# Kernel optimization log

Measured on AMD Instinct MI355X. Metric: run time of the kernel, lower is better.

The kernel has to match this reference:

```python
import jax, jax.numpy as jnp
import numpy as np

D_MODEL = 256
N_HEADS = 8
HEAD_DIM = D_MODEL // N_HEADS


def setup_inputs() -> dict:
    key = jax.random.key(0)
    k1, k2, k3, k4, k5, k6, k7 = jax.random.split(key, 7)
    B, T, N, D = 4, 32, 32, D_MODEL
    x = jax.random.normal(k1, (B, T, N, D), dtype=jnp.float32)
    bias_features = jax.random.normal(k2, (B, T, N, N, D), dtype=jnp.float32)
    # alive mask, mostly True so rows are rarely fully masked
    mask = jax.random.uniform(k3, (B, T, N)) < 0.9
    s = 1.0 / np.sqrt(D)
    w_qkv = jax.random.normal(k4, (D, 3 * D), dtype=jnp.float32) * s
    b_qkv = jnp.zeros((3 * D,), dtype=jnp.float32)
    w_proj = jax.random.normal(k5, (D, D), dtype=jnp.float32) * s
    b_proj = jnp.zeros((D,), dtype=jnp.float32)
    return {"x": x, "bias_features": bias_features, "mask": mask,
            "w_qkv": w_qkv, "b_qkv": b_qkv, "w_proj": w_proj, "b_proj": b_proj}


def reference(x, bias_features, mask, w_qkv, b_qkv, w_proj, b_proj):
    B, T, N, D = x.shape
    H, Dh = N_HEADS, D // N_HEADS
    Bt = B * T
    xf = x.reshape(Bt, N, D)
    qkv = xf @ w_qkv + b_qkv                       # (Bt, N, 3D)
    q, k, v = jnp.split(qkv, 3, axis=-1)
    q = q.reshape(Bt, N, H, Dh)
    k = k.reshape(Bt, N, H, Dh)
    v = v.reshape(Bt, N, H, Dh)
    b_geo = bias_features.reshape(Bt, N, N, H, Dh)
    k_pair = k[:, None] + b_geo                    # (Bt, N, N, H, Dh)
    v_pair = v[:, None] + b_geo
    # scores: (Bt, H, N, N)
    scores = jnp.einsum('bihd,bijhd->bhij', q, k_pair) * (Dh ** -0.5)
    mask_flat = mask.reshape(Bt, 1, 1, N)
    scores = jnp.where(mask_flat, scores, -jnp.inf)
    max_scores = jnp.max(scores, axis=-1, keepdims=True)
    is_nan_row = max_scores == -jnp.inf
    scores_safe = jnp.where(is_nan_row, 0.0, scores)
    attn = jax.nn.softmax(scores_safe, axis=-1)
    attn = jnp.where(is_nan_row, 0.0, attn)
    out = jnp.einsum('bhij,bijhd->bihd', attn, v_pair).reshape(Bt, N, D)
    out = out.reshape(B, T, N, D)
    return out @ w_proj + b_proj
```

## Files before the change

### kernel.cpp

```cpp
#include <hip/hip_runtime.h>
#include <math.h>

typedef __attribute__((ext_vector_type(8))) short bf16x8;
typedef __attribute__((ext_vector_type(4))) short bf16x4;
typedef __attribute__((ext_vector_type(4))) float f32x4;

__device__ inline ushort f2bf(float f) {
    union { float f; uint u; } v; v.f = f;
    uint u = v.u;
    return (ushort)((u + 0x7fff + ((u >> 16) & 1)) >> 16);
}
__device__ inline float bf2f(ushort u) {
    union { uint u; float f; } v; v.u = ((uint)u) << 16; return v.f;
}

template<int BM, int BN, int WGM, int WGN, int MODE>
__global__ __launch_bounds__(WGM * WGN * 64) void gemm_fused(
    const void* __restrict__ Ap, const float* __restrict__ Bw, int ldb,
    const float* __restrict__ bias,
    void* __restrict__ C0, void* __restrict__ C1, void* __restrict__ C2,
    int K, int N)
{
    constexpr int BK = 32;
    constexpr int NT = WGM * WGN * 64;
    constexpr int WM = BM / (WGM * 16);
    constexpr int WN = BN / (WGN * 16);

    __shared__ ushort As[BM * BK];
    __shared__ ushort Bs[BN * BK];

    const int tid = threadIdx.x;
    const int lane = tid & 63, wid = tid >> 6;
    const int wm = wid / WGN, wn = wid % WGN;
    const int row0 = blockIdx.y * BM, col0 = blockIdx.x * BN;
    const int frow = lane & 15, fg = lane >> 4;

    f32x4 acc[WM][WN] = {};

    for (int k0 = 0; k0 < K; k0 += BK) {
        if constexpr (MODE == 0) {
            #pragma unroll
            for (int ci = tid; ci < BM * 8; ci += NT) {
                int r = ci >> 3, kq = ci & 7, g = kq >> 1;
                float4 v = *(const float4*)((const float*)Ap + (size_t)(row0 + r) * K + k0 + kq * 4);
                bf16x4 o;
                o[0] = (short)f2bf(v.x); o[1] = (short)f2bf(v.y);
                o[2] = (short)f2bf(v.z); o[3] = (short)f2bf(v.w);
                *(bf16x4*)&As[r * 32 + ((g ^ ((r >> 1) & 3)) << 3) + (kq & 1) * 4] = o;
            }
        } else {
            #pragma unroll
            for (int ci = tid; ci < BM * 4; ci += NT) {
                int r = ci >> 2, g = ci & 3;
                bf16x8 v = *(const bf16x8*)((const ushort*)Ap + (size_t)(row0 + r) * K + k0 + g * 8);
                *(bf16x8*)&As[r * 32 + ((g ^ ((r >> 1) & 3)) << 3)] = v;
            }
        }
        #pragma unroll
        for (int ci = tid; ci < BN * 8; ci += NT) {
            int kk = ci & 31, n4 = ci >> 5;
            float4 v = *(const float4*)&Bw[(size_t)(k0 + kk) * ldb + col0 + n4 * 4];
            float vv[4] = {v.x, v.y, v.z, v.w};
            #pragma unroll
            for (int e = 0; e < 4; ++e) {
                int n = n4 * 4 + e;
                Bs[n * 32 + (((kk >> 3) ^ ((n >> 1) & 3)) << 3) + (kk & 7)] = f2bf(vv[e]);
            }
        }
        __syncthreads();

        bf16x8 af[WM], bfr[WN];
        #pragma unroll
        for (int m = 0; m < WM; ++m) {
            int r = (wm * WM + m) * 16 + frow;
            af[m] = *(const bf16x8*)&As[r * 32 + ((fg ^ ((r >> 1) & 3)) << 3)];
        }
        #pragma unroll
        for (int n = 0; n < WN; ++n) {
            int r = (wn * WN + n) * 16 + frow;
            bfr[n] = *(const bf16x8*)&Bs[r * 32 + ((fg ^ ((r >> 1) & 3)) << 3)];
        }
        #pragma unroll
        for (int m = 0; m < WM; ++m)
            #pragma unroll
            for (int n = 0; n < WN; ++n)
                acc[m][n] = __builtin_amdgcn_mfma_f32_16x16x32_bf16(
                    af[m], bfr[n], acc[m][n], 0, 0, 0);
        __syncthreads();
    }

    #pragma unroll
    for (int n = 0; n < WN; ++n) {
        int gcol = col0 + (wn * WN + n) * 16 + frow;
        float bv = bias[gcol];
        if constexpr (MODE == 0) {
            int b = gcol >> 8, c = gcol & 255;
            ushort* dst = (b == 0) ? (ushort*)C0 : (b == 1) ? (ushort*)C1 : (ushort*)C2;
            #pragma unroll
            for (int m = 0; m < WM; ++m) {
                int grow0 = row0 + (wm * WM + m) * 16 + fg * 4;
                #pragma unroll
                for (int r = 0; r < 4; ++r)
                    dst[(size_t)(grow0 + r) * 256 + c] = f2bf(acc[m][n][r] + bv);
            }
        } else {
            float* dst = (float*)C0;
            #pragma unroll
            for (int m = 0; m < WM; ++m) {
                int grow0 = row0 + (wm * WM + m) * 16 + fg * 4;
                #pragma unroll
                for (int r = 0; r < 4; ++r)
                    dst[(size_t)(grow0 + r) * N + gcol] = acc[m][n][r] + bv;
            }
        }
    }
}

__global__ __launch_bounds__(256, 4) void relattn_kernel(
    const ushort* __restrict__ qb, const ushort* __restrict__ kb,
    const ushort* __restrict__ vb, const float* __restrict__ bias,
    const int* __restrict__ mask, ushort* __restrict__ attn_out)
{
    const int lane = threadIdx.x & 63;
    const int item = (blockIdx.x << 2) | (threadIdx.x >> 6);
    const int bt = item >> 5;

    const float*  brow  = bias + (size_t)item * 8192;
    const ushort* kbase = kb + (size_t)bt * 8192;
    const ushort* vbase = vb + (size_t)bt * 8192;

    const bool myalive = (mask[bt * 32 + (lane & 31)] != 0);
    const uint amask = (uint)__ballot(myalive);

    bf16x4 q4 = *(const bf16x4*)(qb + (size_t)item * 256 + lane * 4);
    const float qf0 = bf2f((ushort)q4[0]), qf1 = bf2f((ushort)q4[1]);
    const float qf2 = bf2f((ushort)q4[2]), qf3 = bf2f((ushort)q4[3]);

    float m = -1e30f, l = 0.f;
    float o0 = 0.f, o1 = 0.f, o2 = 0.f, o3 = 0.f;

    #pragma unroll 8
    for (int j = 0; j < 32; ++j) {
        float4 b4 = *(const float4*)(brow + j * 256 + lane * 4);
        bf16x4 k4 = *(const bf16x4*)(kbase + j * 256 + lane * 4);
        bf16x4 v4 = *(const bf16x4*)(vbase + j * 256 + lane * 4);

        float s = qf0 * (bf2f((ushort)k4[0]) + b4.x)
                + qf1 * (bf2f((ushort)k4[1]) + b4.y)
                + qf2 * (bf2f((ushort)k4[2]) + b4.z)
                + qf3 * (bf2f((ushort)k4[3]) + b4.w);
        s += __shfl_xor(s, 1);
        s += __shfl_xor(s, 2);
        s += __shfl_xor(s, 4);
        s *= 0.17677669529663687f;

        const bool alive = (amask >> j) & 1;
        const float mn = alive ? fmaxf(m, s) : m;
        const float c = __expf(m - mn);
        const float e = alive ? __expf(s - mn) : 0.f;
        o0 = o0 * c + e * (bf2f((ushort)v4[0]) + b4.x);
        o1 = o1 * c + e * (bf2f((ushort)v4[1]) + b4.y);
        o2 = o2 * c + e * (bf2f((ushort)v4[2]) + b4.z);
        o3 = o3 * c + e * (bf2f((ushort)v4[3]) + b4.w);
        l = l * c + e;
        m = mn;
    }

    const float rl = (l > 0.f) ? 1.f / l : 0.f;
    bf16x4 rr;
    rr[0] = (short)f2bf(o0 * rl);
    rr[1] = (short)f2bf(o1 * rl);
    rr[2] = (short)f2bf(o2 * rl);
    rr[3] = (short)f2bf(o3 * rl);
    *(bf16x4*)(attn_out + (size_t)item * 256 + lane * 4) = rr;
}

extern "C" void kernel_launch(void* const* d_in, const int* in_sizes, int n_in,
                              void* d_out, int out_size, void* d_ws, size_t ws_size,
                              hipStream_t stream) {
    const float* x      = (const float*)d_in[0];
    const float* bias_f = (const float*)d_in[1];
    const int*   mask   = (const int*)d_in[2];
    const float* w_qkv  = (const float*)d_in[3];
    const float* b_qkv  = (const float*)d_in[4];
    const float* w_proj = (const float*)d_in[5];
    const float* b_proj = (const float*)d_in[6];
    float* out = (float*)d_out;

    ushort* qb = (ushort*)d_ws;
    ushort* kb = qb + (size_t)4096 * 256;
    ushort* vb = kb + (size_t)4096 * 256;
    ushort* ao = vb + (size_t)4096 * 256;

    gemm_fused<64, 64, 2, 2, 0><<<dim3(12, 64), 256, 0, stream>>>(
        x, w_qkv, 768, b_qkv, qb, kb, vb, 256, 768);

    relattn_kernel<<<1024, 256, 0, stream>>>(qb, kb, vb, bias_f, mask, ao);

    gemm_fused<32, 64, 1, 4, 1><<<dim3(4, 128), 256, 0, stream>>>(
        ao, w_proj, 256, b_proj, out, nullptr, nullptr, 256, 256);
}
```

Before: 55.89 us.

## Interleave K/V storage and drop online-softmax max tracking in relattn

```diff
diff --git a/kernel.cpp b/kernel.cpp
--- a/kernel.cpp
+++ b/kernel.cpp
@@ -18,7 +18,7 @@
 __global__ __launch_bounds__(WGM * WGN * 64) void gemm_fused(
     const void* __restrict__ Ap, const float* __restrict__ Bw, int ldb,
     const float* __restrict__ bias,
-    void* __restrict__ C0, void* __restrict__ C1, void* __restrict__ C2,
+    void* __restrict__ C0, void* __restrict__ C1,
     int K, int N)
 {
     constexpr int BK = 32;
@@ -94,14 +94,18 @@
         int gcol = col0 + (wn * WN + n) * 16 + frow;
         float bv = bias[gcol];
         if constexpr (MODE == 0) {
-            int b = gcol >> 8, c = gcol & 255;
-            ushort* dst = (b == 0) ? (ushort*)C0 : (b == 1) ? (ushort*)C1 : (ushort*)C2;
+            int bq = gcol >> 8, c = gcol & 255;
             #pragma unroll
             for (int m = 0; m < WM; ++m) {
                 int grow0 = row0 + (wm * WM + m) * 16 + fg * 4;
                 #pragma unroll
-                for (int r = 0; r < 4; ++r)
-                    dst[(size_t)(grow0 + r) * 256 + c] = f2bf(acc[m][n][r] + bv);
+                for (int r = 0; r < 4; ++r) {
+                    ushort val = f2bf(acc[m][n][r] + bv);
+                    size_t row = (size_t)(grow0 + r);
+                    if (bq == 0)      ((ushort*)C0)[row * 256 + c] = val;
+                    else if (bq == 1) ((ushort*)C1)[row * 512 + c * 2] = val;
+                    else              ((ushort*)C1)[row * 512 + c * 2 + 1] = val;
+                }
             }
         } else {
             float* dst = (float*)C0;
@@ -117,61 +121,66 @@
 }
 
 __global__ __launch_bounds__(256, 4) void relattn_kernel(
-    const ushort* __restrict__ qb, const ushort* __restrict__ kb,
-    const ushort* __restrict__ vb, const float* __restrict__ bias,
-    const int* __restrict__ mask, ushort* __restrict__ attn_out)
+    const ushort* __restrict__ qb, const ushort* __restrict__ kv,
+    const float* __restrict__ bias, const int* __restrict__ mask,
+    ushort* __restrict__ attn_out)
 {
     const int lane = threadIdx.x & 63;
     const int item = (blockIdx.x << 2) | (threadIdx.x >> 6);
     const int bt = item >> 5;
 
-    const float*  brow  = bias + (size_t)item * 8192;
-    const ushort* kbase = kb + (size_t)bt * 8192;
-    const ushort* vbase = vb + (size_t)bt * 8192;
+    const float*  brow   = bias + (size_t)item * 8192;
+    const ushort* kvbase = kv + (size_t)bt * 16384;
 
     const bool myalive = (mask[bt * 32 + (lane & 31)] != 0);
     const uint amask = (uint)__ballot(myalive);
 
     bf16x4 q4 = *(const bf16x4*)(qb + (size_t)item * 256 + lane * 4);
-    const float qf0 = bf2f((ushort)q4[0]), qf1 = bf2f((ushort)q4[1]);
-    const float qf2 = bf2f((ushort)q4[2]), qf3 = bf2f((ushort)q4[3]);
-
-    float m = -1e30f, l = 0.f;
-    float o0 = 0.f, o1 = 0.f, o2 = 0.f, o3 = 0.f;
-
-    #pragma unroll 8
+    const float qf0 = bf2f((ushort)q4[0]) * 0.17677669529663687f;
+    const float qf1 = bf2f((ushort)q4[1]) * 0.17677669529663687f;
+    const float qf2 = bf2f((ushort)q4[2]) * 0.17677669529663687f;
+    const float qf3 = bf2f((ushort)q4[3]) * 0.17677669529663687f;
+
+    float la = 0.f, lb = 0.f;
+    float o0a = 0.f, o1a = 0.f, o2a = 0.f, o3a = 0.f;
+    float o0b = 0.f, o1b = 0.f, o2b = 0.f, o3b = 0.f;
+
+    #pragma unroll
     for (int j = 0; j < 32; ++j) {
         float4 b4 = *(const float4*)(brow + j * 256 + lane * 4);
-        bf16x4 k4 = *(const bf16x4*)(kbase + j * 256 + lane * 4);
-        bf16x4 v4 = *(const bf16x4*)(vbase + j * 256 + lane * 4);
-
-        float s = qf0 * (bf2f((ushort)k4[0]) + b4.x)
-                + qf1 * (bf2f((ushort)k4[1]) + b4.y)
-                + qf2 * (bf2f((ushort)k4[2]) + b4.z)
-                + qf3 * (bf2f((ushort)k4[3]) + b4.w);
+        bf16x8 kv8 = *(const bf16x8*)(kvbase + j * 512 + lane * 8);
+
+        float s = qf0 * (bf2f((ushort)kv8[0]) + b4.x)
+                + qf1 * (bf2f((ushort)kv8[2]) + b4.y)
+                + qf2 * (bf2f((ushort)kv8[4]) + b4.z)
+                + qf3 * (bf2f((ushort)kv8[6]) + b4.w);
         s += __shfl_xor(s, 1);
         s += __shfl_xor(s, 2);
         s += __shfl_xor(s, 4);
-        s *= 0.17677669529663687f;
-
-        const bool alive = (amask >> j) & 1;
-        const float mn = alive ? fmaxf(m, s) : m;
-        const float c = __expf(m - mn);
-        const float e = alive ? __expf(s - mn) : 0.f;
-        o0 = o0 * c + e * (bf2f((ushort)v4[0]) + b4.x);
-        o1 = o1 * c + e * (bf2f((ushort)v4[1]) + b4.y);
-        o2 = o2 * c + e * (bf2f((ushort)v4[2]) + b4.z);
-        o3 = o3 * c + e * (bf2f((ushort)v4[3]) + b4.w);
-        l = l * c + e;
-        m = mn;
+
+        const float e = ((amask >> j) & 1) ? __expf(s) : 0.f;
+        if (j & 1) {
+            lb += e;
+            o0b += e * (bf2f((ushort)kv8[1]) + b4.x);
+            o1b += e * (bf2f((ushort)kv8[3]) + b4.y);
+            o2b += e * (bf2f((ushort)kv8[5]) + b4.z);
+            o3b += e * (bf2f((ushort)kv8[7]) + b4.w);
+        } else {
+            la += e;
+            o0a += e * (bf2f((ushort)kv8[1]) + b4.x);
+            o1a += e * (bf2f((ushort)kv8[3]) + b4.y);
+            o2a += e * (bf2f((ushort)kv8[5]) + b4.z);
+            o3a += e * (bf2f((ushort)kv8[7]) + b4.w);
+        }
     }
 
+    const float l = la + lb;
     const float rl = (l > 0.f) ? 1.f / l : 0.f;
     bf16x4 rr;
-    rr[0] = (short)f2bf(o0 * rl);
-    rr[1] = (short)f2bf(o1 * rl);
-    rr[2] = (short)f2bf(o2 * rl);
-    rr[3] = (short)f2bf(o3 * rl);
+    rr[0] = (short)f2bf((o0a + o0b) * rl);
+    rr[1] = (short)f2bf((o1a + o1b) * rl);
+    rr[2] = (short)f2bf((o2a + o2b) * rl);
+    rr[3] = (short)f2bf((o3a + o3b) * rl);
     *(bf16x4*)(attn_out + (size_t)item * 256 + lane * 4) = rr;
 }
 
@@ -188,15 +197,14 @@
     float* out = (float*)d_out;
 
     ushort* qb = (ushort*)d_ws;
-    ushort* kb = qb + (size_t)4096 * 256;
-    ushort* vb = kb + (size_t)4096 * 256;
-    ushort* ao = vb + (size_t)4096 * 256;
+    ushort* kv = qb + (size_t)4096 * 256;
+    ushort* ao = kv + (size_t)4096 * 512;
 
     gemm_fused<64, 64, 2, 2, 0><<<dim3(12, 64), 256, 0, stream>>>(
-        x, w_qkv, 768, b_qkv, qb, kb, vb, 256, 768);
-
-    relattn_kernel<<<1024, 256, 0, stream>>>(qb, kb, vb, bias_f, mask, ao);
+        x, w_qkv, 768, b_qkv, qb, kv, 256, 768);
+
+    relattn_kernel<<<1024, 256, 0, stream>>>(qb, kv, bias_f, mask, ao);
 
     gemm_fused<32, 64, 1, 4, 1><<<dim3(4, 128), 256, 0, stream>>>(
-        ao, w_proj, 256, b_proj, out, nullptr, nullptr, 256, 256);
-}
+        ao, w_proj, 256, b_proj, out, nullptr, 256, 256);
+}
```

New measurement: 129.0 us. 2.31x slower.
